# Kernel optimization log

Hardware: AMD Instinct MI355X
Metric: run time of the kernel (lower is better)

Reference implementation:

```python
import jax, jax.numpy as jnp
import jax.lax as lax
import numpy as np

X_NUM = 512
Y_NUM = 512
GRID = 1.0 / 512.0
MIN_X = 0.0
MIN_Y = 0.0
N_POINTS = 400000
BATCH = 4
NUM_CLASSES = 20


def setup_inputs():
    key = jax.random.key(0)
    ks = jax.random.split(key, 32)
    # rows 0/1: x,y coords in [0,1) so they land inside the 512x512 grid; rows 2-5: features
    xy = jax.random.uniform(ks[0], (2, N_POINTS), jnp.float32, 0.0, 1.0 - 1e-6)
    feat = jax.random.normal(ks[1], (4, N_POINTS), jnp.float32) * 0.5
    points = jnp.concatenate([xy, feat], 0)
    batch_ids = jax.random.randint(ks[2], (N_POINTS,), 0, BATCH, jnp.int32)
    inp = {"batch_ids": batch_ids, "points": points, "batch_size": BATCH}

    def lin(k, o, i):
        return jax.random.normal(k, (o, i), jnp.float32) * (1.0 / np.sqrt(i))

    ki = 3
    # pointwise conv1d stacks: (name, out_ch, in_ch)
    for name, o, i in [("0", 16, 6), ("1", 16, 16), ("v0", 16, 18), ("v1", 16, 32), ("2", 32, 32)]:
        inp["w" + name] = lin(ks[ki], o, i); ki += 1
        inp["b" + name] = jnp.zeros((o,), jnp.float32)
        inp["s" + name] = jax.random.uniform(ks[ki], (o,), jnp.float32, 0.5, 1.5); ki += 1
        inp["t" + name] = jax.random.normal(ks[ki], (o,), jnp.float32) * 0.1; ki += 1
    inp["w2d"] = jax.random.normal(ks[ki], (4, 32, 32, 3, 3), jnp.float32) * (1.0 / np.sqrt(32 * 9)); ki += 1
    inp["b2d"] = jnp.zeros((4, 32), jnp.float32)
    inp["s2d"] = jax.random.uniform(ks[ki], (4, 32), jnp.float32, 0.5, 1.5); ki += 1
    inp["t2d"] = jax.random.normal(ks[ki], (4, 32), jnp.float32) * 0.1; ki += 1
    inp["w3"] = lin(ks[ki], NUM_CLASSES, 64); ki += 1
    inp["b3"] = jnp.zeros((NUM_CLASSES,), jnp.float32)
    return inp


def _pconv(x, w, b, s, t):
    # 1x1 conv1d + BatchNorm(inference affine) + ReLU; x: [Cin, N]
    return jax.nn.relu((w @ x + b[:, None]) * s[:, None] + t[:, None])


def _scatter_max(v, gids, n):
    # v: [C, N] -> [C, n]; empty segments filled with 0 (torch_scatter fill_value=0,
    # and all scattered values here are post-ReLU >= 0)
    seg = jax.ops.segment_max(v.T, gids, num_segments=n).T
    return jnp.where(jnp.isneginf(seg), 0.0, seg)


def _bilinear(img, ix, iy):
    # grid_sample(align_corners=False, padding zeros) in pixel coords; img: [C, H, W]
    C, H, W = img.shape
    x0 = jnp.floor(ix); y0 = jnp.floor(iy)
    wx = ix - x0; wy = iy - y0
    x0i = x0.astype(jnp.int32); y0i = y0.astype(jnp.int32)

    def tap(yi, xi):
        valid = ((yi >= 0) & (yi < H) & (xi >= 0) & (xi < W)).astype(img.dtype)
        return img[:, jnp.clip(yi, 0, H - 1), jnp.clip(xi, 0, W - 1)] * valid

    return (tap(y0i, x0i) * (1 - wx) * (1 - wy) + tap(y0i, x0i + 1) * wx * (1 - wy)
            + tap(y0i + 1, x0i) * (1 - wx) * wy + tap(y0i + 1, x0i + 1) * wx * wy)


def _forward(batch_ids, points, batch_size, w0, b0, s0, t0, w1, b1, s1, t1,
             wv0, bv0, sv0, tv0, wv1, bv1, sv1, tv1, w2, b2, s2, t2,
             w2d, b2d, s2d, t2d, w3, b3):
    x_g = jnp.floor((points[0] - MIN_X) / GRID).astype(jnp.int32)
    y_g = jnp.floor((points[1] - MIN_Y) / GRID).astype(jnp.int32)
    gids = batch_ids.astype(jnp.int32) * (X_NUM * Y_NUM) + y_g * X_NUM + x_g
    grid_num = batch_size * Y_NUM * X_NUM

    h = _pconv(points, w0, b0, s0, t0)       # [16, N]
    h = _pconv(h, w1, b1, s1, t1)            # [16, N]
    vx = (x_g.astype(jnp.float32) + 0.5) * GRID + MIN_X
    vy = (y_g.astype(jnp.float32) + 0.5) * GRID + MIN_Y
    h = jnp.concatenate([h, (points[0] - vx)[None], (points[1] - vy)[None]], 0)  # [18, N]

    # VFE blocks: pointwise conv -> scatter_max over voxel ids -> gather back -> concat
    o = _pconv(h, wv0, bv0, sv0, tv0)        # [16, N]
    h = jnp.concatenate([o, _scatter_max(o, gids, grid_num)[:, gids]], 0)  # [32, N]
    o = _pconv(h, wv1, bv1, sv1, tv1)        # [16, N]
    h = jnp.concatenate([o, _scatter_max(o, gids, grid_num)[:, gids]], 0)  # [32, N]

    point0 = _pconv(h, w2, b2, s2, t2)       # [32, N]
    grid = _scatter_max(point0, gids, grid_num)
    grid = grid.reshape(32, batch_size, Y_NUM, X_NUM).transpose(1, 0, 2, 3)  # [B,32,Y,X]

    for i in range(4):
        p = 1 if i == 0 else 2
        grid = lax.conv_general_dilated(grid, w2d[i], (1, 1), ((p, p), (p, p)),
                                        rhs_dilation=(p, p),
                                        dimension_numbers=("NCHW", "OIHW", "NCHW"))
        grid = jax.nn.relu((grid + b2d[i][None, :, None, None]) * s2d[i][None, :, None, None]
                           + t2d[i][None, :, None, None])

    # interpolate (grid_sample) back to points; pixel coords reduce to (x-MIN)/GRID - 1
    img = grid.transpose(1, 0, 2, 3).reshape(32, batch_size * Y_NUM, X_NUM)
    ix = (points[0] - MIN_X) / GRID - 1.0
    iy = (points[1] - MIN_Y) / GRID - 1.0 + batch_ids.astype(jnp.float32) * Y_NUM
    point1 = _bilinear(img, ix, iy)          # [32, N]

    point = jnp.concatenate([point0, point1], 0)  # [64, N]
    return w3 @ point + b3[:, None]               # [num_classes, N]


def reference(batch_ids, points, batch_size, w0, b0, s0, t0, w1, b1, s1, t1,
              wv0, bv0, sv0, tv0, wv1, bv1, sv1, tv1, w2, b2, s2, t2,
              w2d, b2d, s2d, t2d, w3, b3):
    return _forward(batch_ids, points, batch_size, w0, b0, s0, t0, w1, b1, s1, t1,
                    wv0, bv0, sv0, tv0, wv1, bv1, sv1, tv1, w2, b2, s2, t2,
                    w2d, b2d, s2d, t2d, w3, b3)
```

## Files before the change

### kernel.cpp

```cpp
#include <hip/hip_runtime.h>
#include <hip/hip_bf16.h>
#include <hip/hip_fp16.h>

#define N_PTS 400000
#define XN 512
#define YN 512
#define BATCHN 4
#define VOX (XN*YN)
#define GRID_NUM (BATCHN*VOX)

typedef unsigned long long u64;
typedef __attribute__((ext_vector_type(8))) _Float16 f16x8;
typedef __attribute__((ext_vector_type(4))) float f32x4;

static __device__ __forceinline__ float relu_(float x){ return fmaxf(x, 0.0f); }
static __device__ __forceinline__ int voxel_id(float px, float py, int b){
    int xg = (int)floorf(px*512.0f);
    int yg = (int)floorf(py*512.0f);
    return b*VOX + yg*XN + xg;
}

static __device__ __forceinline__ u64 packh4(const float* v){
    u64 r = 0;
    #pragma unroll
    for (int j=0;j<4;j++){
        unsigned short h = __half_as_ushort(__float2half_rn(v[j]));
        r |= (u64)h << (16*j);
    }
    return r;
}
static __device__ __forceinline__ void unpackh4(u64 w, float* o){
    #pragma unroll
    for (int j=0;j<4;j++)
        o[j] = __half2float(__ushort_as_half((unsigned short)(w >> (16*j))));
}
static __device__ __forceinline__ u64 pkmax4(u64 a, u64 b){
    u64 r = 0;
    #pragma unroll
    for (int j=0;j<4;j++){
        u64 x = (a >> (16*j)) & 0xFFFFull;
        u64 y = (b >> (16*j)) & 0xFFFFull;
        r |= (x > y ? x : y) << (16*j);
    }
    return r;
}

__global__ void kZero(float4* __restrict__ p, int n4){
    int i = blockIdx.x*256 + threadIdx.x;
    const float4 z = make_float4(0.f,0.f,0.f,0.f);
    for (; i < n4; i += gridDim.x*256) p[i] = z;
}

__global__ void kDiag(float* __restrict__ o, int n, float v){
    int i = blockIdx.x*256 + threadIdx.x;
    for (; i < n; i += gridDim.x*256) o[i] = v;
}

__global__ void kWprep(const float* __restrict__ W32, _Float16* __restrict__ wf){
    int idx = blockIdx.x*256 + threadIdx.x;
    if (idx >= 4*9216) return;
    int L = idx / 9216, r = idx % 9216;
    int j = r & 7, ln = (r>>3) & 63, rest = r >> 9;
    int t = rest >> 1, nt = rest & 1;
    int ic = (ln>>4)*8 + j, oc = nt*16 + (ln&15);
    wf[idx] = (_Float16)W32[(size_t)L*9216 + ((size_t)oc*32 + ic)*9 + t];
}

__global__ void kHist(const int* __restrict__ bid, const float* __restrict__ pts,
                      unsigned* __restrict__ offs, int* __restrict__ gids)
{
    int i = blockIdx.x*256 + threadIdx.x;
    if (i >= N_PTS) return;
    int gid = voxel_id(pts[i], pts[N_PTS+i], bid[i]);
    gids[i] = gid;
    atomicAdd(&offs[gid], 1u);
}

__global__ void kScan1(unsigned* __restrict__ offs, unsigned* __restrict__ partials)
{
    __shared__ unsigned sa[256], sb[256];
    const int t = threadIdx.x;
    const int g = blockIdx.x*256 + t;
    unsigned v = offs[g];
    sa[t] = v;
    __syncthreads();
    unsigned* src = sa; unsigned* dst = sb;
    #pragma unroll
    for (int d=1; d<256; d<<=1){
        dst[t] = src[t] + ((t>=d) ? src[t-d] : 0u);
        __syncthreads();
        unsigned* tmp = src; src = dst; dst = tmp;
    }
    unsigned incl = src[t];
    offs[g] = incl - v;
    if (t == 255) partials[blockIdx.x] = incl;
}
__global__ void kScan2(unsigned* __restrict__ partials)
{
    __shared__ unsigned sa[256], sb[256];
    const int t = threadIdx.x;
    unsigned loc[16]; unsigned sum = 0;
    #pragma unroll
    for (int j=0;j<16;j++){ loc[j] = partials[t*16+j]; sum += loc[j]; }
    sa[t] = sum;
    __syncthreads();
    unsigned* src = sa; unsigned* dst = sb;
    #pragma unroll
    for (int d=1; d<256; d<<=1){
        dst[t] = src[t] + ((t>=d) ? src[t-d] : 0u);
        __syncthreads();
        unsigned* tmp = src; src = dst; dst = tmp;
    }
    unsigned run = src[t] - sum;
    #pragma unroll
    for (int j=0;j<16;j++){ unsigned c = loc[j]; partials[t*16+j] = run; run += c; }
}
__global__ void kScan3(unsigned* __restrict__ offs, const unsigned* __restrict__ partials)
{
    int g = blockIdx.x*256 + threadIdx.x;
    offs[g] += partials[blockIdx.x];
}

__global__ void kA(const int* __restrict__ bid, const float* __restrict__ pts,
                   const int* __restrict__ gids,
                   const float* __restrict__ w0, const float* __restrict__ b0,
                   const float* __restrict__ s0, const float* __restrict__ t0,
                   const float* __restrict__ w1, const float* __restrict__ b1,
                   const float* __restrict__ s1, const float* __restrict__ t1,
                   const float* __restrict__ wv0, const float* __restrict__ bv0,
                   const float* __restrict__ sv0, const float* __restrict__ tv0,
                   u64* __restrict__ obufA, unsigned* __restrict__ offs,
                   int* __restrict__ sGid, unsigned* __restrict__ inv)
{
    int i = blockIdx.x*256 + threadIdx.x;
    if (i >= N_PTS) return;
    float p[6];
    #pragma unroll
    for (int r=0;r<6;r++) p[r] = pts[r*N_PTS+i];
    int xg = (int)floorf(p[0]*512.0f);
    int yg = (int)floorf(p[1]*512.0f);

    float h0[16];
    #pragma unroll
    for (int o=0;o<16;o++){
        float a = b0[o];
        #pragma unroll
        for (int k=0;k<6;k++) a = fmaf(w0[o*6+k], p[k], a);
        h0[o] = relu_(fmaf(a, s0[o], t0[o]));
    }
    float h1[16];
    #pragma unroll
    for (int o=0;o<16;o++){
        float a = b1[o];
        #pragma unroll
        for (int k=0;k<16;k++) a = fmaf(w1[o*16+k], h0[k], a);
        h1[o] = relu_(fmaf(a, s1[o], t1[o]));
    }
    float dx = p[0] - ((float)xg + 0.5f)*(1.0f/512.0f);
    float dy = p[1] - ((float)yg + 0.5f)*(1.0f/512.0f);
    float vv[16];
    #pragma unroll
    for (int o=0;o<16;o++){
        float a = bv0[o];
        #pragma unroll
        for (int k=0;k<16;k++) a = fmaf(wv0[o*18+k], h1[k], a);
        a = fmaf(wv0[o*18+16], dx, a);
        a = fmaf(wv0[o*18+17], dy, a);
        vv[o] = relu_(fmaf(a, sv0[o], tv0[o]));
    }
    int gid = gids[i];
    unsigned pos = atomicAdd(&offs[gid], 1u);
    u64* op = obufA + (size_t)pos*4;
    #pragma unroll
    for (int q=0;q<4;q++) op[q] = packh4(&vv[q*4]);
    sGid[pos] = gid;
    inv[i] = pos;
}

__global__ void kSegMax(const unsigned* __restrict__ offs,
                        const u64* __restrict__ src, u64* __restrict__ dst)
{
    int v = blockIdx.x*256 + threadIdx.x;
    unsigned s = v ? offs[v-1] : 0u;
    unsigned e = offs[v];
    if (e <= s) return;
    u64 m0=0,m1=0,m2=0,m3=0;
    for (unsigned p=s; p<e; ++p){
        const u64* q = src + (size_t)p*4;
        m0 = pkmax4(m0, q[0]); m1 = pkmax4(m1, q[1]);
        m2 = pkmax4(m2, q[2]); m3 = pkmax4(m3, q[3]);
    }
    u64* d = dst + (size_t)v*4;
    d[0]=m0; d[1]=m1; d[2]=m2; d[3]=m3;
}

__global__ void kGridMax(const unsigned* __restrict__ offs,
                         const u64* __restrict__ src, u64* __restrict__ dst)
{
    int v = blockIdx.x*256 + threadIdx.x;
    unsigned s = v ? offs[v-1] : 0u;
    unsigned e = offs[v];
    u64 m[8];
    #pragma unroll
    for (int q=0;q<8;q++) m[q] = 0ull;
    for (unsigned p=s; p<e; ++p){
        const u64* q = src + (size_t)p*8;
        #pragma unroll
        for (int j=0;j<8;j++) m[j] = pkmax4(m[j], q[j]);
    }
    u64* d = dst + (size_t)v*8;
    #pragma unroll
    for (int q=0;q<8;q++) d[q] = m[q];
}

__global__ void kB(const int* __restrict__ sGid,
                   const float* __restrict__ w, const float* __restrict__ bb,
                   const float* __restrict__ ss, const float* __restrict__ tt,
                   const u64* __restrict__ obufA, const u64* __restrict__ seg0,
                   u64* __restrict__ obufB)
{
    int j = blockIdx.x*256 + threadIdx.x;
    if (j >= N_PTS) return;
    int gid = sGid[j];
    float h[32];
    const u64* ap = obufA + (size_t)j*4;
    #pragma unroll
    for (int q=0;q<4;q++) unpackh4(ap[q], &h[q*4]);
    const u64* sp = seg0 + (size_t)gid*4;
    #pragma unroll
    for (int q=0;q<4;q++) unpackh4(sp[q], &h[16+q*4]);

    float o[16];
    #pragma unroll
    for (int c=0;c<16;c++){
        float a = bb[c];
        #pragma unroll
        for (int k=0;k<32;k++) a = fmaf(w[c*32+k], h[k], a);
        o[c] = relu_(fmaf(a, ss[c], tt[c]));
    }
    u64* op = obufB + (size_t)j*4;
    #pragma unroll
    for (int q=0;q<4;q++) op[q] = packh4(&o[q*4]);
}

__global__ void kC(const int* __restrict__ sGid,
                   const float* __restrict__ w, const float* __restrict__ bb,
                   const float* __restrict__ ss, const float* __restrict__ tt,
                   const u64* __restrict__ obufB, const u64* __restrict__ seg1,
                   u64* __restrict__ pbuf)
{
    int j = blockIdx.x*256 + threadIdx.x;
    if (j >= N_PTS) return;
    int gid = sGid[j];
    float h[32];
    const u64* ap = obufB + (size_t)j*4;
    #pragma unroll
    for (int q=0;q<4;q++) unpackh4(ap[q], &h[q*4]);
    const u64* sp = seg1 + (size_t)gid*4;
    #pragma unroll
    for (int q=0;q<4;q++) unpackh4(sp[q], &h[16+q*4]);

    float p0v[32];
    #pragma unroll
    for (int c=0;c<32;c++){
        float a = bb[c];
        #pragma unroll
        for (int k=0;k<32;k++) a = fmaf(w[c*32+k], h[k], a);
        p0v[c] = relu_(fmaf(a, ss[c], tt[c]));
    }
    u64* pp = pbuf + (size_t)j*8;
    #pragma unroll
    for (int q=0;q<8;q++) pp[q] = packh4(&p0v[q*4]);
}

template<int P>
__global__ __launch_bounds__(256,4) void convM(
    const _Float16* __restrict__ in, _Float16* __restrict__ out,
    const f16x8* __restrict__ wfrag, const float* __restrict__ bb,
    const float* __restrict__ ss, const float* __restrict__ tt)
{
    constexpr int TW = 32, TH = 8;
    constexpr int TIW = TW + 2*P, TIH = TH + 2*P;
    __shared__ uint4 sA[TIH*TIW*5];
    const int tid = threadIdx.x;
    const int lane = tid & 63, wv = tid >> 6;
    const int x0 = blockIdx.x*TW, y0 = blockIdx.y*TH, bz = blockIdx.z;
    const _Float16* inB = in + (size_t)bz*VOX*32;

    for (int u = tid; u < TIH*TIW*4; u += 256){
        int g = u & 3;
        int pxr = u >> 2;
        int px = pxr % TIW, r = pxr / TIW;
        int gy = y0 - P + r, gx = x0 - P + px;
        uint4 v = make_uint4(0,0,0,0);
        if ((unsigned)gy < 512u && (unsigned)gx < 512u)
            v = *(const uint4*)(inB + (((size_t)gy*512 + gx)*32 + g*8));
        sA[(r*TIW + px)*5 + g] = v;
    }
    __syncthreads();

    const f16x8* pA = (const f16x8*)sA;
    const int aoff = (lane&15)*5 + (lane>>4);
    const int rowbase = wv*2;

    f32x4 acc[4][2];
    #pragma unroll
    for (int m=0;m<4;m++){ acc[m][0]=(f32x4)0.f; acc[m][1]=(f32x4)0.f; }

    #pragma unroll
    for (int t=0;t<9;t++){
        const int ky = t/3, kx = t%3;
        f16x8 b0 = wfrag[(t*2+0)*64 + lane];
        f16x8 b1 = wfrag[(t*2+1)*64 + lane];
        #pragma unroll
        for (int m=0;m<4;m++){
            int r = rowbase + (m>>1) + ky*P;
            int pxb = (m&1)*16 + kx*P;
            f16x8 a = pA[(r*TIW + pxb)*5 + aoff];
            acc[m][0] = __builtin_amdgcn_mfma_f32_16x16x32_f16(b0, a, acc[m][0], 0,0,0);
            acc[m][1] = __builtin_amdgcn_mfma_f32_16x16x32_f16(b1, a, acc[m][1], 0,0,0);
        }
    }

    float bn[2][4], sn[2][4], tn[2][4];
    #pragma unroll
    for (int n=0;n<2;n++){
        int ocb = n*16 + (lane>>4)*4;
        #pragma unroll
        for (int r=0;r<4;r++){ bn[n][r]=bb[ocb+r]; sn[n][r]=ss[ocb+r]; tn[n][r]=tt[ocb+r]; }
    }
    _Float16* outB = out + (size_t)bz*VOX*32;
    #pragma unroll
    for (int m=0;m<4;m++){
        int y  = y0 + rowbase + (m>>1);
        int px = x0 + (m&1)*16 + (lane&15);
        #pragma unroll
        for (int n=0;n<2;n++){
            unsigned h[4];
            #pragma unroll
            for (int r=0;r<4;r++){
                float v = relu_(fmaf(acc[m][n][r] + bn[n][r], sn[n][r], tn[n][r]));
                h[r] = (unsigned)__half_as_ushort(__float2half_rn(v));
            }
            uint2 val = make_uint2(h[0] | (h[1]<<16), h[2] | (h[3]<<16));
            *(uint2*)(outB + ((size_t)y*512 + px)*32 + n*16 + (lane>>4)*4) = val;
        }
    }
}

__global__ __launch_bounds__(256) void kFinal(
    const int* __restrict__ bid, const float* __restrict__ pts,
    const unsigned* __restrict__ inv, const u64* __restrict__ pbuf,
    const _Float16* __restrict__ gridH,
    const float* __restrict__ w3, const float* __restrict__ b3,
    float* __restrict__ outp)
{
    int i = blockIdx.x*256 + threadIdx.x;
    if (i >= N_PTS) return;
    float px = pts[i], py = pts[N_PTS+i];
    int b = bid[i];
    unsigned j = inv[i];

    const u64* pp = pbuf + (size_t)j*8;
    u64 pk[8];
    #pragma unroll
    for (int q=0;q<8;q++) pk[q] = pp[q];

    float ix = px*512.0f - 1.0f;
    float iy = py*512.0f - 1.0f + (float)(b*512);
    float x0f = floorf(ix), y0f = floorf(iy);
    float wx = ix - x0f, wy = iy - y0f;
    int x0 = (int)x0f, y0 = (int)y0f;

    uint4 tv[4][4];
    float wgt[4];
    #pragma unroll
    for (int t=0;t<4;t++){
        int yi = y0 + (t>>1), xi = x0 + (t&1);
        bool ok = (yi >= 0) & (yi < BATCHN*YN) & (xi >= 0) & (xi < XN);
        wgt[t] = (((t>>1)? wy : 1.0f-wy) * ((t&1)? wx : 1.0f-wx)) * (ok ? 1.0f : 0.0f);
        int cy = min(max(yi,0), BATCHN*YN-1), cx = min(max(xi,0), XN-1);
        const uint4* tp = (const uint4*)(gridH + ((size_t)cy*XN + cx)*32);
        #pragma unroll
        for (int q=0;q<4;q++) tv[t][q] = tp[q];
    }

    float p1[32];
    #pragma unroll
    for (int c=0;c<32;c++) p1[c] = 0.f;
    #pragma unroll
    for (int t=0;t<4;t++){
        float w = wgt[t];
        #pragma unroll
        for (int q=0;q<4;q++){
            const unsigned int* vu = (const unsigned int*)&tv[t][q];
            #pragma unroll
            for (int e=0;e<4;e++){
                float lo = __half2float(__ushort_as_half((unsigned short)(vu[e] & 0xFFFF)));
                float hi = __half2float(__ushort_as_half((unsigned short)(vu[e] >> 16)));
                p1[q*8 + e*2 + 0] = fmaf(w, lo, p1[q*8 + e*2 + 0]);
                p1[q*8 + e*2 + 1] = fmaf(w, hi, p1[q*8 + e*2 + 1]);
            }
        }
    }

    float p0[32];
    #pragma unroll
    for (int q=0;q<8;q++) unpackh4(pk[q], &p0[q*4]);

    #pragma unroll
    for (int k=0;k<20;k++){
        float a = b3[k];
        #pragma unroll
        for (int c=0;c<32;c++) a = fmaf(w3[k*64+c], p0[c], a);
        #pragma unroll
        for (int c=0;c<32;c++) a = fmaf(w3[k*64+32+c], p1[c], a);
        outp[(size_t)k*N_PTS + i] = a;
    }
}

extern "C" void kernel_launch(void* const* d_in, const int* in_sizes, int n_in,
                              void* d_out, int out_size, void* d_ws, size_t ws_size,
                              hipStream_t stream)
{
    const int*   bid = (const int*)  d_in[0];
    const float* pts = (const float*)d_in[1];
    const float* w0  = (const float*)d_in[3];
    const float* b0  = (const float*)d_in[4];
    const float* s0  = (const float*)d_in[5];
    const float* t0  = (const float*)d_in[6];
    const float* w1  = (const float*)d_in[7];
    const float* b1  = (const float*)d_in[8];
    const float* s1  = (const float*)d_in[9];
    const float* t1  = (const float*)d_in[10];
    const float* wv0 = (const float*)d_in[11];
    const float* bv0 = (const float*)d_in[12];
    const float* sv0 = (const float*)d_in[13];
    const float* tv0 = (const float*)d_in[14];
    const float* wv1 = (const float*)d_in[15];
    const float* bv1 = (const float*)d_in[16];
    const float* sv1 = (const float*)d_in[17];
    const float* tv1 = (const float*)d_in[18];
    const float* w2  = (const float*)d_in[19];
    const float* b2  = (const float*)d_in[20];
    const float* s2  = (const float*)d_in[21];
    const float* t2  = (const float*)d_in[22];
    const float* w2d = (const float*)d_in[23];
    const float* b2d = (const float*)d_in[24];
    const float* s2d = (const float*)d_in[25];
    const float* t2d = (const float*)d_in[26];
    const float* w3  = (const float*)d_in[27];
    const float* b3  = (const float*)d_in[28];

    const size_t MB = 1024*1024;
    const size_t NEED = 192*MB;
    if (ws_size < NEED){
        kDiag<<<512,256,0,stream>>>((float*)d_out, out_size, (float)(ws_size>>20));
        return;
    }

    char* ws = (char*)d_ws;
    u64*      gridV    = (u64*)ws;
    _Float16* ping     = (_Float16*)ws;
    _Float16* pong     = (_Float16*)(ws + 64*MB);
    u64*      seg0     = (u64*)(ws + 64*MB);
    u64*      seg1     = (u64*)(ws + 96*MB);
    unsigned* offs     = (unsigned*)(ws + 128*MB);
    unsigned* partials = (unsigned*)(ws + 132*MB);
    int*      sGid     = (int*)(ws + 133*MB);
    int*      gids     = (int*)(ws + 135*MB);
    unsigned* inv      = (unsigned*)(ws + 137*MB);
    u64*      obufA    = (u64*)(ws + 139*MB);
    u64*      obufB    = (u64*)(ws + 152*MB);
    u64*      pbuf     = (u64*)(ws + 165*MB);
    _Float16* wfrag    = (_Float16*)(ws + 191*MB);

    kZero<<<256,256,0,stream>>>((float4*)offs, (int)(GRID_NUM*4/16));
    kWprep<<<144,256,0,stream>>>(w2d, wfrag);

    const int nb = (N_PTS + 255)/256;
    const int nv = GRID_NUM/256;

    kHist <<<nb,256,0,stream>>>(bid, pts, offs, gids);
    kScan1<<<nv,256,0,stream>>>(offs, partials);
    kScan2<<<1,256,0,stream>>>(partials);
    kScan3<<<nv,256,0,stream>>>(offs, partials);

    kA<<<nb,256,0,stream>>>(bid, pts, gids, w0,b0,s0,t0, w1,b1,s1,t1,
                            wv0,bv0,sv0,tv0, obufA, offs, sGid, inv);
    kSegMax<<<nv,256,0,stream>>>(offs, obufA, seg0);
    kB<<<nb,256,0,stream>>>(sGid, wv1,bv1,sv1,tv1, obufA, seg0, obufB);
    kSegMax<<<nv,256,0,stream>>>(offs, obufB, seg1);
    kC<<<nb,256,0,stream>>>(sGid, w2,b2,s2,t2, obufB, seg1, pbuf);
    kGridMax<<<nv,256,0,stream>>>(offs, pbuf, gridV);

    dim3 cgrid(XN/32, YN/8, BATCHN);
    const f16x8* wf = (const f16x8*)wfrag;
    convM<1><<<cgrid,256,0,stream>>>(ping, pong, wf + 0*1152, b2d + 0,  s2d + 0,  t2d + 0);
    convM<2><<<cgrid,256,0,stream>>>(pong, ping, wf + 1*1152, b2d + 32, s2d + 32, t2d + 32);
    convM<2><<<cgrid,256,0,stream>>>(ping, pong, wf + 2*1152, b2d + 64, s2d + 64, t2d + 64);
    convM<2><<<cgrid,256,0,stream>>>(pong, ping, wf + 3*1152, b2d + 96, s2d + 96, t2d + 96);

    kFinal<<<nb,256,0,stream>>>(bid, pts, inv, pbuf, ping, w3, b3, (float*)d_out);
}
```

Measured before the change: 344.3 us.

## Run final bilinear+classifier in voxel-sorted order, then permute output

The final kernel now processes points in their voxel-sorted position, so pbuf reads are contiguous and grid bilinear reads are spatially coherent. Coordinates are stashed in sorted order during kA, and the batch id is recovered from the sorted gid. A new permutation kernel scatters the 20 logits back to the original point order. This trades random gathers in the heavy kernel for an extra 32 MB intermediate write/read and one more launch.

```diff
diff --git a/kernel.cpp b/kernel.cpp
--- a/kernel.cpp
+++ b/kernel.cpp
@@ -130,7 +130,8 @@
                    const float* __restrict__ wv0, const float* __restrict__ bv0,
                    const float* __restrict__ sv0, const float* __restrict__ tv0,
                    u64* __restrict__ obufA, unsigned* __restrict__ offs,
-                   int* __restrict__ sGid, unsigned* __restrict__ inv)
+                   int* __restrict__ sGid, unsigned* __restrict__ inv,
+                   float2* __restrict__ sCrd)
 {
     int i = blockIdx.x*256 + threadIdx.x;
     if (i >= N_PTS) return;
@@ -175,6 +176,7 @@
     for (int q=0;q<4;q++) op[q] = packh4(&vv[q*4]);
     sGid[pos] = gid;
     inv[i] = pos;
+    sCrd[pos] = make_float2(p[0], p[1]);
 }
 
 __global__ void kSegMax(const unsigned* __restrict__ offs,
@@ -348,26 +350,24 @@
     }
 }
 
-__global__ __launch_bounds__(256) void kFinal(
-    const int* __restrict__ bid, const float* __restrict__ pts,
-    const unsigned* __restrict__ inv, const u64* __restrict__ pbuf,
-    const _Float16* __restrict__ gridH,
+__global__ __launch_bounds__(256) void kFinalS(
+    const int* __restrict__ sGid, const float2* __restrict__ sCrd,
+    const u64* __restrict__ pbuf, const _Float16* __restrict__ gridH,
     const float* __restrict__ w3, const float* __restrict__ b3,
-    float* __restrict__ outp)
-{
-    int i = blockIdx.x*256 + threadIdx.x;
-    if (i >= N_PTS) return;
-    float px = pts[i], py = pts[N_PTS+i];
-    int b = bid[i];
-    unsigned j = inv[i];
+    float* __restrict__ outS)
+{
+    int j = blockIdx.x*256 + threadIdx.x;
+    if (j >= N_PTS) return;
+    float2 crd = sCrd[j];
+    int b = sGid[j] >> 18;
 
     const u64* pp = pbuf + (size_t)j*8;
     u64 pk[8];
     #pragma unroll
     for (int q=0;q<8;q++) pk[q] = pp[q];
 
-    float ix = px*512.0f - 1.0f;
-    float iy = py*512.0f - 1.0f + (float)(b*512);
+    float ix = crd.x*512.0f - 1.0f;
+    float iy = crd.y*512.0f - 1.0f + (float)(b*512);
     float x0f = floorf(ix), y0f = floorf(iy);
     float wx = ix - x0f, wy = iy - y0f;
     int x0 = (int)x0f, y0 = (int)y0f;
@@ -408,6 +408,7 @@
     #pragma unroll
     for (int q=0;q<8;q++) unpackh4(pk[q], &p0[q*4]);
 
+    float* os = outS + (size_t)j*20;
     #pragma unroll
     for (int k=0;k<20;k++){
         float a = b3[k];
@@ -415,8 +416,23 @@
         for (int c=0;c<32;c++) a = fmaf(w3[k*64+c], p0[c], a);
         #pragma unroll
         for (int c=0;c<32;c++) a = fmaf(w3[k*64+32+c], p1[c], a);
-        outp[(size_t)k*N_PTS + i] = a;
-    }
+        os[k] = a;
+    }
+}
+
+__global__ __launch_bounds__(256) void kPerm(
+    const unsigned* __restrict__ inv, const float* __restrict__ outS,
+    float* __restrict__ outp)
+{
+    int i = blockIdx.x*256 + threadIdx.x;
+    if (i >= N_PTS) return;
+    unsigned j = inv[i];
+    const float* os = outS + (size_t)j*20;
+    float v[20];
+    #pragma unroll
+    for (int k=0;k<20;k++) v[k] = os[k];
+    #pragma unroll
+    for (int k=0;k<20;k++) outp[(size_t)k*N_PTS + i] = v[k];
 }
 
 extern "C" void kernel_launch(void* const* d_in, const int* in_sizes, int n_in,
@@ -453,7 +469,7 @@
     const float* b3  = (const float*)d_in[28];
 
     const size_t MB = 1024*1024;
-    const size_t NEED = 192*MB;
+    const size_t NEED = 228*MB;
     if (ws_size < NEED){
         kDiag<<<512,256,0,stream>>>((float*)d_out, out_size, (float)(ws_size>>20));
         return;
@@ -474,6 +490,8 @@
     u64*      obufB    = (u64*)(ws + 152*MB);
     u64*      pbuf     = (u64*)(ws + 165*MB);
     _Float16* wfrag    = (_Float16*)(ws + 191*MB);
+    float2*   sCrd     = (float2*)(ws + 192*MB);
+    float*    outS     = (float*)(ws + 196*MB);
 
     kZero<<<256,256,0,stream>>>((float4*)offs, (int)(GRID_NUM*4/16));
     kWprep<<<144,256,0,stream>>>(w2d, wfrag);
@@ -487,7 +505,7 @@
     kScan3<<<nv,256,0,stream>>>(offs, partials);
 
     kA<<<nb,256,0,stream>>>(bid, pts, gids, w0,b0,s0,t0, w1,b1,s1,t1,
-                            wv0,bv0,sv0,tv0, obufA, offs, sGid, inv);
+                            wv0,bv0,sv0,tv0, obufA, offs, sGid, inv, sCrd);
     kSegMax<<<nv,256,0,stream>>>(offs, obufA, seg0);
     kB<<<nb,256,0,stream>>>(sGid, wv1,bv1,sv1,tv1, obufA, seg0, obufB);
     kSegMax<<<nv,256,0,stream>>>(offs, obufB, seg1);
@@ -501,5 +519,6 @@
     convM<2><<<cgrid,256,0,stream>>>(ping, pong, wf + 2*1152, b2d + 64, s2d + 64, t2d + 64);
     convM<2><<<cgrid,256,0,stream>>>(pong, ping, wf + 3*1152, b2d + 96, s2d + 96, t2d + 96);
 
-    kFinal<<<nb,256,0,stream>>>(bid, pts, inv, pbuf, ping, w3, b3, (float*)d_out);
-}
+    kFinalS<<<nb,256,0,stream>>>(sGid, sCrd, pbuf, ping, w3, b3, outS);
+    kPerm<<<nb,256,0,stream>>>(inv, outS, (float*)d_out);
+}
```

After: 390.7 us. +13.5%, slower.
